# Kernel tuning notes

Measured on AMD Instinct MI355X. Metric: run time of the kernel, lower is better.

Reference implementation:

```python
import jax, jax.numpy as jnp
import numpy as np

H = W = 128
N_RAYS = H * W
N_SAMPLES = 2 ** 21
NUM_LEVELS = 12
BASE_RES = 16
PER_LEVEL_SCALE = 2.0
TABLE_SIZE = 2 ** 19
LEVEL_DIM = 2
RENDER_STEP = 0.005
BG_COLOR = 1.0
PRIMES = (1, 2654435761, 805459861)


def hash_encode(x01, table):
    """Multi-resolution hash-grid encoding. x01: [N,3] in [0,1]; table: [L,T,D]."""
    L, T, D = table.shape
    mask = np.uint32(T - 1)
    feats = []
    for l in range(L):
        res = int(np.ceil(BASE_RES * PER_LEVEL_SCALE ** l))
        pos = x01 * (res - 1)            # [N,3]
        p0f = jnp.floor(pos)
        f = pos - p0f                    # trilinear fractions
        p0 = p0f.astype(jnp.uint32)
        acc = jnp.zeros((x01.shape[0], D), dtype=table.dtype)
        for cx in range(2):
            for cy in range(2):
                for cz in range(2):
                    ix = p0[:, 0] + jnp.uint32(cx)
                    iy = p0[:, 1] + jnp.uint32(cy)
                    iz = p0[:, 2] + jnp.uint32(cz)
                    idx = ((ix * jnp.uint32(PRIMES[0]))
                           ^ (iy * jnp.uint32(PRIMES[1]))
                           ^ (iz * jnp.uint32(PRIMES[2]))) & mask
                    w = ((f[:, 0] if cx else 1.0 - f[:, 0])
                         * (f[:, 1] if cy else 1.0 - f[:, 1])
                         * (f[:, 2] if cz else 1.0 - f[:, 2]))
                    acc = acc + w[:, None] * table[l][idx]
        feats.append(acc)
    return jnp.concatenate(feats, axis=-1)  # [N, L*D]


@jax.custom_vjp
def trunc_exp(x):
    return jnp.exp(x)

def _te_fwd(x):
    return jnp.exp(x), x

def _te_bwd(x, g):
    return (g * jnp.exp(jnp.clip(x, -15.0, 15.0)),)

trunc_exp.defvjp(_te_fwd, _te_bwd)


def setup_inputs() -> dict:
    key = jax.random.key(0)
    ks = jax.random.split(key, 12)
    rays_o = 0.1 * jax.random.normal(ks[0], (N_RAYS, 3), jnp.float32)
    rd = jax.random.normal(ks[1], (N_RAYS, 3), jnp.float32)
    rays_d = rd / jnp.linalg.norm(rd, axis=-1, keepdims=True)
    t_starts = 0.01 + 1.5 * jax.random.uniform(ks[2], (N_SAMPLES,), jnp.float32)
    t_ends = t_starts + RENDER_STEP
    ray_indices = jnp.sort(jax.random.randint(ks[3], (N_SAMPLES,), 0, N_RAYS)).astype(jnp.int32)
    table_density = 1e-2 * jax.random.normal(ks[4], (NUM_LEVELS, TABLE_SIZE, LEVEL_DIM), jnp.float32)
    table_color = 1e-2 * jax.random.normal(ks[5], (NUM_LEVELS, TABLE_SIZE, LEVEL_DIM), jnp.float32)
    d_in = NUM_LEVELS * LEVEL_DIM
    w_d1 = jax.random.normal(ks[6], (d_in, 32), jnp.float32) / np.sqrt(d_in)
    w_d2 = jax.random.normal(ks[7], (32, 1), jnp.float32) / np.sqrt(32)
    w_c1 = jax.random.normal(ks[8], (d_in, 32), jnp.float32) / np.sqrt(d_in)
    w_c2 = jax.random.normal(ks[9], (32, 3), jnp.float32) / np.sqrt(32)
    return {"rays_o": rays_o, "rays_d": rays_d, "t_starts": t_starts, "t_ends": t_ends,
            "ray_indices": ray_indices, "table_density": table_density, "table_color": table_color,
            "w_d1": w_d1, "w_d2": w_d2, "w_c1": w_c1, "w_c2": w_c2}


def reference(rays_o, rays_d, t_starts, t_ends, ray_indices,
              table_density, table_color, w_d1, w_d2, w_c1, w_c2):
    # sample positions along rays
    t_mid = 0.5 * (t_starts + t_ends)
    xs = rays_o[ray_indices] + rays_d[ray_indices] * t_mid[:, None]     # [N,3]
    x01 = jnp.clip((xs + 1.0) * 0.5, 0.0, 1.0)                          # aabb [-1,1] -> [0,1]

    # density branch: hash encode -> tiny MLP -> trunc_exp
    fd = hash_encode(x01, table_density)                                # [N,24]
    sigma = trunc_exp(jax.nn.relu(fd @ w_d1) @ w_d2)[:, 0]              # [N]

    # color branch: hash encode -> tiny MLP -> sigmoid
    fc = hash_encode(x01, table_color)
    rgb = jax.nn.sigmoid(jax.nn.relu(fc @ w_c1) @ w_c2)                 # [N,3]

    # render_weight_from_density (segment-wise exclusive transmittance)
    s = sigma * (t_ends - t_starts)                                     # [N], >= 0
    e = jnp.cumsum(s) - s                                               # exclusive cumsum, nondecreasing
    e_start = jax.ops.segment_min(e, ray_indices, num_segments=N_RAYS)
    trans = jnp.exp(-(e - e_start[ray_indices]))
    alphas = 1.0 - jnp.exp(-s)
    weights = alphas * trans                                            # [N]

    # accumulate_along_rays
    color = jax.ops.segment_sum(weights[:, None] * rgb, ray_indices, num_segments=N_RAYS)  # [R,3]
    acc = jax.ops.segment_sum(weights, ray_indices, num_segments=N_RAYS)                   # [R]
    color = color + (1.0 - acc)[:, None] * BG_COLOR
    color = jnp.clip(color, 0.0, 1.0).reshape(H, W, 3).transpose(2, 0, 1)
    alpha = jnp.clip(acc, 0.0, 1.0).reshape(H, W)
    return color, alpha
```

## Files before the change

kernel.cpp:

```cpp
#include <hip/hip_runtime.h>
#include <hip/hip_fp16.h>
#include <cstdint>
#include <cstddef>

#define HW_NRAYS 16384
#define NSAMP    (1 << 21)
#define NLEV     12
#define TSZ      (1 << 19)
#define TMASK    (TSZ - 1)
#define DIN      24
#define HDIM     32
#define WS_TAB_QWORDS (NLEV * TSZ)
#define WS_TAB_BYTES  ((size_t)WS_TAB_QWORDS * 8)
#define WS_FEAT_BYTES ((size_t)NLEV * NSAMP * 8)
#define PRIME1 2654435761u
#define PRIME2 805459861u

__device__ __forceinline__ float clamp01f(float v) { return fminf(fmaxf(v, 0.f), 1.f); }

__device__ __forceinline__ uint32_t rne_bf16_lo(uint32_t u) {
    return (u + 0x7fffu + ((u >> 16) & 1u)) >> 16;
}
__device__ __forceinline__ float bf_lo(uint32_t v) { return __uint_as_float(v << 16); }
__device__ __forceinline__ float bf_hi(uint32_t v) { return __uint_as_float(v & 0xffff0000u); }

__global__ __launch_bounds__(256)
void ngp_pack_tables(const float2* __restrict__ tab_d,
                     const float2* __restrict__ tab_c,
                     uint2* __restrict__ ws_tab)
{
    const int stride = gridDim.x * blockDim.x;
    for (int i = blockIdx.x * blockDim.x + threadIdx.x; i < WS_TAB_QWORDS; i += stride) {
        const float2 d = tab_d[i];
        const float2 c = tab_c[i];
        const uint32_t w0 = rne_bf16_lo(__float_as_uint(d.x)) | (rne_bf16_lo(__float_as_uint(d.y)) << 16);
        const uint32_t w1 = rne_bf16_lo(__float_as_uint(c.x)) | (rne_bf16_lo(__float_as_uint(c.y)) << 16);
        ws_tab[i] = make_uint2(w0, w1);
    }
}

union H2U { __half2 h2; uint32_t u; };
union F4H2 { float4 f4; __half2 h2[4]; };

__device__ __forceinline__ void level_hashes(float x, float y, float z, int l,
                                             uint32_t* __restrict__ h,
                                             float* __restrict__ w)
{
    const float res1 = (float)((16 << l) - 1);
    const float px = x * res1, py = y * res1, pz = z * res1;
    const float fxf = floorf(px), fyf = floorf(py), fzf = floorf(pz);
    const uint32_t ix = (uint32_t)fxf, iy = (uint32_t)fyf, iz = (uint32_t)fzf;
    const float fx = px - fxf, fy = py - fyf, fz = pz - fzf;
    const uint32_t hx0 = ix, hx1 = ix + 1u;
    const uint32_t hy0 = iy * PRIME1, hy1 = hy0 + PRIME1;
    const uint32_t hz0 = iz * PRIME2, hz1 = hz0 + PRIME2;
    #pragma unroll
    for (int c = 0; c < 8; ++c) {
        h[c] = ((((c & 1) ? hx1 : hx0) ^ ((c & 2) ? hy1 : hy0) ^ ((c & 4) ? hz1 : hz0)) & TMASK);
        w[c] = ((c & 1) ? fx : 1.f - fx) * ((c & 2) ? fy : 1.f - fy) * ((c & 4) ? fz : 1.f - fz);
    }
}

__global__ __launch_bounds__(256)
void ngp_encode(const float* __restrict__ rays_o,
                const float* __restrict__ rays_d,
                const float* __restrict__ t_starts,
                const float* __restrict__ t_ends,
                const int*   __restrict__ ray_idx,
                const uint2* __restrict__ ws_tab,
                uint2* __restrict__ feat)
{
    const int l = blockIdx.x >> 13;
    const int i = ((blockIdx.x & 8191) << 8) | threadIdx.x;

    const int ridx = ray_idx[i];
    const float tm = 0.5f * (t_starts[i] + t_ends[i]);
    const float x = clamp01f((rays_o[3 * ridx + 0] + rays_d[3 * ridx + 0] * tm + 1.f) * 0.5f);
    const float y = clamp01f((rays_o[3 * ridx + 1] + rays_d[3 * ridx + 1] * tm + 1.f) * 0.5f);
    const float z = clamp01f((rays_o[3 * ridx + 2] + rays_d[3 * ridx + 2] * tm + 1.f) * 0.5f);

    const float res1 = (float)((16 << l) - 1);
    const float px = x * res1, py = y * res1, pz = z * res1;
    const float fxf = floorf(px), fyf = floorf(py), fzf = floorf(pz);
    const uint32_t ix = (uint32_t)fxf, iy = (uint32_t)fyf, iz = (uint32_t)fzf;
    const float fx = px - fxf, fy = py - fyf, fz = pz - fzf;
    const float wx0 = 1.f - fx, wx1 = fx;

    const uint32_t hy0 = iy * PRIME1, hy1 = hy0 + PRIME1;
    const uint32_t hz0 = iz * PRIME2, hz1 = hz0 + PRIME2;

    uint32_t hyz[4];
    float    wyz[4];
    hyz[0] = hy0 ^ hz0; wyz[0] = (1.f - fy) * (1.f - fz);
    hyz[1] = hy1 ^ hz0; wyz[1] = fy * (1.f - fz);
    hyz[2] = hy0 ^ hz1; wyz[2] = (1.f - fy) * fz;
    hyz[3] = hy1 ^ hz1; wyz[3] = fy * fz;

    const uint4* pairs = (const uint4*)(ws_tab + (size_t)l * TSZ);

    float a0 = 0.f, a1 = 0.f, b0 = 0.f, b1 = 0.f;
    #pragma unroll
    for (int k = 0; k < 4; ++k) {
        const uint32_t h0 = (ix        ^ hyz[k]) & TMASK;
        const uint32_t h1 = ((ix + 1u) ^ hyz[k]) & TMASK;
        uint4 q0 = pairs[h0 >> 1];
        uint4 q1 = q0;
        if ((h1 >> 1) != (h0 >> 1)) q1 = pairs[h1 >> 1];
        const uint32_t e0x = (h0 & 1u) ? q0.z : q0.x;
        const uint32_t e0y = (h0 & 1u) ? q0.w : q0.y;
        const uint32_t e1x = (h1 & 1u) ? q1.z : q1.x;
        const uint32_t e1y = (h1 & 1u) ? q1.w : q1.y;
        const float w0 = wx0 * wyz[k], w1 = wx1 * wyz[k];
        a0 += w0 * bf_lo(e0x) + w1 * bf_lo(e1x);
        a1 += w0 * bf_hi(e0x) + w1 * bf_hi(e1x);
        b0 += w0 * bf_lo(e0y) + w1 * bf_lo(e1y);
        b1 += w0 * bf_hi(e0y) + w1 * bf_hi(e1y);
    }

    H2U fD, fC;
    fD.h2 = __floats2half2_rn(a0, a1);
    fC.h2 = __floats2half2_rn(b0, b1);
    const unsigned long long packed = (unsigned long long)fD.u | ((unsigned long long)fC.u << 32);
    __builtin_nontemporal_store(packed, (unsigned long long*)(feat + (size_t)l * NSAMP + i));
}

#define PROC_LEVEL2(FA, FB, LIDX)                                                \
    do {                                                                         \
        H2U fDa, fCa, fDb, fCb;                                                  \
        fDa.u = (FA).x; fCa.u = (FA).y; fDb.u = (FB).x; fCb.u = (FB).y;          \
        const __half2 a0A = __low2half2(fDa.h2), a1A = __high2half2(fDa.h2);     \
        const __half2 b0A = __low2half2(fCa.h2), b1A = __high2half2(fCa.h2);     \
        const __half2 a0B = __low2half2(fDb.h2), a1B = __high2half2(fDb.h2);     \
        const __half2 b0B = __low2half2(fCb.h2), b1B = __high2half2(fCb.h2);     \
        const F4H2* wd0 = (const F4H2*)(s_wd1h + (2 * (LIDX) + 0) * 16);         \
        const F4H2* wd1 = (const F4H2*)(s_wd1h + (2 * (LIDX) + 1) * 16);         \
        const F4H2* wc0 = (const F4H2*)(s_wc1h + (2 * (LIDX) + 0) * 16);         \
        const F4H2* wc1 = (const F4H2*)(s_wc1h + (2 * (LIDX) + 1) * 16);         \
        _Pragma("unroll")                                                        \
        for (int q = 0; q < 4; ++q) {                                            \
            F4H2 u0 = wd0[q], u1 = wd1[q], v0 = wc0[q], v1 = wc1[q];             \
            _Pragma("unroll")                                                    \
            for (int p = 0; p < 4; ++p) {                                        \
                hbD2A[q * 4 + p] = __hfma2(a0A, u0.h2[p],                        \
                                     __hfma2(a1A, u1.h2[p], hbD2A[q * 4 + p]));  \
                hbC2A[q * 4 + p] = __hfma2(b0A, v0.h2[p],                        \
                                     __hfma2(b1A, v1.h2[p], hbC2A[q * 4 + p]));  \
                hbD2B[q * 4 + p] = __hfma2(a0B, u0.h2[p],                        \
                                     __hfma2(a1B, u1.h2[p], hbD2B[q * 4 + p]));  \
                hbC2B[q * 4 + p] = __hfma2(b0B, v0.h2[p],                        \
                                     __hfma2(b1B, v1.h2[p], hbC2B[q * 4 + p]));  \
            }                                                                    \
        }                                                                        \
    } while (0)

#define PROC_LEVEL(FV, LIDX)                                                     \
    do {                                                                         \
        H2U fDu, fCu; fDu.u = (FV).x; fCu.u = (FV).y;                            \
        const __half2 a0h = __low2half2(fDu.h2), a1h = __high2half2(fDu.h2);     \
        const __half2 b0h = __low2half2(fCu.h2), b1h = __high2half2(fCu.h2);     \
        const F4H2* wd0 = (const F4H2*)(s_wd1h + (2 * (LIDX) + 0) * 16);         \
        const F4H2* wd1 = (const F4H2*)(s_wd1h + (2 * (LIDX) + 1) * 16);         \
        const F4H2* wc0 = (const F4H2*)(s_wc1h + (2 * (LIDX) + 0) * 16);         \
        const F4H2* wc1 = (const F4H2*)(s_wc1h + (2 * (LIDX) + 1) * 16);         \
        _Pragma("unroll")                                                        \
        for (int q = 0; q < 4; ++q) {                                            \
            F4H2 u0 = wd0[q], u1 = wd1[q], v0 = wc0[q], v1 = wc1[q];             \
            _Pragma("unroll")                                                    \
            for (int p = 0; p < 4; ++p) {                                        \
                hbD2[q * 4 + p] = __hfma2(a0h, u0.h2[p],                         \
                                    __hfma2(a1h, u1.h2[p], hbD2[q * 4 + p]));    \
                hbC2[q * 4 + p] = __hfma2(b0h, v0.h2[p],                         \
                                    __hfma2(b1h, v1.h2[p], hbC2[q * 4 + p]));    \
            }                                                                    \
        }                                                                        \
    } while (0)

__global__ __launch_bounds__(256)
void ngp_render_feat(const float* __restrict__ t_starts,
                     const float* __restrict__ t_ends,
                     const int*   __restrict__ ray_idx,
                     const uint2* __restrict__ feat,
                     const float* __restrict__ w_d1,
                     const float* __restrict__ w_d2,
                     const float* __restrict__ w_c1,
                     const float* __restrict__ w_c2,
                     float* __restrict__ out)
{
    __shared__ __align__(16) __half2 s_wd1h[DIN * 16];
    __shared__ __align__(16) __half2 s_wc1h[DIN * 16];
    __shared__ __align__(16) float   s_wd2[HDIM];
    __shared__ __align__(16) float   s_wc2[HDIM * 3];

    const int tid = threadIdx.x;
    for (int idx = tid; idx < DIN * 16; idx += 256) {
        const int k = idx >> 4, j2 = idx & 15;
        s_wd1h[idx] = __floats2half2_rn(w_d1[k * HDIM + 2 * j2], w_d1[k * HDIM + 2 * j2 + 1]);
        s_wc1h[idx] = __floats2half2_rn(w_c1[k * HDIM + 2 * j2], w_c1[k * HDIM + 2 * j2 + 1]);
    }
    if (tid < HDIM) s_wd2[tid] = w_d2[tid];
    if (tid < HDIM * 3) s_wc2[tid] = w_c2[tid];
    __syncthreads();

    const int lane = tid & 63;
    const int r = blockIdx.x * 4 + (tid >> 6);

    int lo = 0, hi = NSAMP;
    while (lo < hi) { int m = (lo + hi) >> 1; if (ray_idx[m] < r) lo = m + 1; else hi = m; }
    const int start = lo;
    hi = NSAMP;
    while (lo < hi) { int m = (lo + hi) >> 1; if (ray_idx[m] <= r) lo = m + 1; else hi = m; }
    const int end = lo;

    float carry = 0.f, accw = 0.f, cr = 0.f, cg = 0.f, cb = 0.f;

    for (int base = start; base < end; base += 128) {
        const bool vA = (base + lane) < end;
        const bool vB = (base + 64 + lane) < end;
        const int iA = min(base + lane, end - 1);
        const int iB = min(base + 64 + lane, end - 1);

        const float dtA = t_ends[iA] - t_starts[iA];
        const float dtB = t_ends[iB] - t_starts[iB];

        __half2 hbD2A[16], hbC2A[16], hbD2B[16], hbC2B[16];
        #pragma unroll
        for (int j = 0; j < 16; ++j) {
            hbD2A[j] = __floats2half2_rn(0.f, 0.f);
            hbC2A[j] = __floats2half2_rn(0.f, 0.f);
            hbD2B[j] = __floats2half2_rn(0.f, 0.f);
            hbC2B[j] = __floats2half2_rn(0.f, 0.f);
        }

        const uint2* fplA = feat + iA;
        const uint2* fplB = feat + iB;
        #pragma unroll 1
        for (int lg = 0; lg < NLEV; lg += 4) {
            const uint2 fA0 = fplA[(size_t)(lg + 0) * NSAMP];
            const uint2 fA1 = fplA[(size_t)(lg + 1) * NSAMP];
            const uint2 fA2 = fplA[(size_t)(lg + 2) * NSAMP];
            const uint2 fA3 = fplA[(size_t)(lg + 3) * NSAMP];
            const uint2 fB0 = fplB[(size_t)(lg + 0) * NSAMP];
            const uint2 fB1 = fplB[(size_t)(lg + 1) * NSAMP];
            const uint2 fB2 = fplB[(size_t)(lg + 2) * NSAMP];
            const uint2 fB3 = fplB[(size_t)(lg + 3) * NSAMP];
            PROC_LEVEL2(fA0, fB0, lg + 0);
            PROC_LEVEL2(fA1, fB1, lg + 1);
            PROC_LEVEL2(fA2, fB2, lg + 2);
            PROC_LEVEL2(fA3, fB3, lg + 3);
        }

        float sDA = 0.f, sDB = 0.f;
        #pragma unroll
        for (int j = 0; j < 16; ++j) {
            const float2 fa = __half22float2(hbD2A[j]);
            const float2 fb = __half22float2(hbD2B[j]);
            sDA += fmaxf(fa.x, 0.f) * s_wd2[2 * j] + fmaxf(fa.y, 0.f) * s_wd2[2 * j + 1];
            sDB += fmaxf(fb.x, 0.f) * s_wd2[2 * j] + fmaxf(fb.y, 0.f) * s_wd2[2 * j + 1];
        }
        const float svA = vA ? __expf(sDA) * dtA : 0.f;
        const float svB = vB ? __expf(sDB) * dtB : 0.f;

        float prA = 0.f, pgA = 0.f, pbA = 0.f, prB = 0.f, pgB = 0.f, pbB = 0.f;
        #pragma unroll
        for (int j = 0; j < 16; ++j) {
            const float2 fa = __half22float2(hbC2A[j]);
            const float2 fb = __half22float2(hbC2B[j]);
            const float a0 = fmaxf(fa.x, 0.f), a1 = fmaxf(fa.y, 0.f);
            const float c0 = fmaxf(fb.x, 0.f), c1 = fmaxf(fb.y, 0.f);
            const float w00 = s_wc2[3 * (2 * j) + 0], w10 = s_wc2[3 * (2 * j + 1) + 0];
            const float w01 = s_wc2[3 * (2 * j) + 1], w11 = s_wc2[3 * (2 * j + 1) + 1];
            const float w02 = s_wc2[3 * (2 * j) + 2], w12 = s_wc2[3 * (2 * j + 1) + 2];
            prA += a0 * w00 + a1 * w10;  prB += c0 * w00 + c1 * w10;
            pgA += a0 * w01 + a1 * w11;  pgB += c0 * w01 + c1 * w11;
            pbA += a0 * w02 + a1 * w12;  pbB += c0 * w02 + c1 * w12;
        }
        const float RA = 1.f / (1.f + __expf(-prA));
        const float GA = 1.f / (1.f + __expf(-pgA));
        const float BA = 1.f / (1.f + __expf(-pbA));
        const float RB = 1.f / (1.f + __expf(-prB));
        const float GB = 1.f / (1.f + __expf(-pgB));
        const float BB = 1.f / (1.f + __expf(-pbB));

        float inclA = svA;
        #pragma unroll
        for (int off = 1; off < 64; off <<= 1) {
            float t = __shfl_up(inclA, off);
            if (lane >= off) inclA += t;
        }
        const float eA = carry + (inclA - svA);
        const float wA = vA ? (1.f - __expf(-svA)) * __expf(-eA) : 0.f;
        const float totalA = __shfl(inclA, 63);

        float inclB = svB;
        #pragma unroll
        for (int off = 1; off < 64; off <<= 1) {
            float t = __shfl_up(inclB, off);
            if (lane >= off) inclB += t;
        }
        const float eB = carry + totalA + (inclB - svB);
        const float wB = vB ? (1.f - __expf(-svB)) * __expf(-eB) : 0.f;
        carry += totalA + __shfl(inclB, 63);

        accw += wA + wB;
        cr += wA * RA + wB * RB;
        cg += wA * GA + wB * GB;
        cb += wA * BA + wB * BB;
    }

    #pragma unroll
    for (int off = 32; off > 0; off >>= 1) {
        accw += __shfl_down(accw, off);
        cr   += __shfl_down(cr, off);
        cg   += __shfl_down(cg, off);
        cb   += __shfl_down(cb, off);
    }

    if (lane == 0) {
        const float bgw = 1.f - accw;
        out[0 * HW_NRAYS + r] = clamp01f(cr + bgw);
        out[1 * HW_NRAYS + r] = clamp01f(cg + bgw);
        out[2 * HW_NRAYS + r] = clamp01f(cb + bgw);
        out[3 * HW_NRAYS + r] = clamp01f(accw);
    }
}

__global__ __launch_bounds__(256, 6)
void ngp_render_fast(const float* __restrict__ rays_o,
                     const float* __restrict__ rays_d,
                     const float* __restrict__ t_starts,
                     const float* __restrict__ t_ends,
                     const int*   __restrict__ ray_idx,
                     const uint2* __restrict__ ws_tab,
                     const float* __restrict__ w_d1,
                     const float* __restrict__ w_d2,
                     const float* __restrict__ w_c1,
                     const float* __restrict__ w_c2,
                     float* __restrict__ out)
{
    __shared__ __align__(16) __half2 s_wd1h[DIN * 16];
    __shared__ __align__(16) __half2 s_wc1h[DIN * 16];
    __shared__ __align__(16) float   s_wd2[HDIM];
    __shared__ __align__(16) float   s_wc2[HDIM * 3];
    __shared__ __align__(16) uint2   s_feat[4 * NLEV * 64];

    const int tid = threadIdx.x;
    for (int idx = tid; idx < DIN * 16; idx += 256) {
        const int k = idx >> 4, j2 = idx & 15;
        s_wd1h[idx] = __floats2half2_rn(w_d1[k * HDIM + 2 * j2], w_d1[k * HDIM + 2 * j2 + 1]);
        s_wc1h[idx] = __floats2half2_rn(w_c1[k * HDIM + 2 * j2], w_c1[k * HDIM + 2 * j2 + 1]);
    }
    if (tid < HDIM) s_wd2[tid] = w_d2[tid];
    if (tid < HDIM * 3) s_wc2[tid] = w_c2[tid];
    __syncthreads();

    const int lane = tid & 63;
    const int wv = tid >> 6;
    const int r = blockIdx.x * 4 + wv;
    uint2* const feat = s_feat + wv * (NLEV * 64) + lane;

    int lo = 0, hi = NSAMP;
    while (lo < hi) { int m = (lo + hi) >> 1; if (ray_idx[m] < r) lo = m + 1; else hi = m; }
    const int start = lo;
    hi = NSAMP;
    while (lo < hi) { int m = (lo + hi) >> 1; if (ray_idx[m] <= r) lo = m + 1; else hi = m; }
    const int end = lo;

    const float ox = rays_o[3 * r + 0], oy = rays_o[3 * r + 1], oz = rays_o[3 * r + 2];
    const float dx = rays_d[3 * r + 0], dy = rays_d[3 * r + 1], dz = rays_d[3 * r + 2];

    float carry = 0.f, accw = 0.f, cr = 0.f, cg = 0.f, cb = 0.f;

    for (int base = start; base < end; base += 64) {
        const int i = base + lane;
        const bool valid = i < end;
        float sv = 0.f, R = 0.f, G = 0.f, B = 0.f;
        if (valid) {
            const float ts = t_starts[i], te = t_ends[i];
            const float tm = 0.5f * (ts + te);
            const float x01x = clamp01f((ox + dx * tm + 1.f) * 0.5f);
            const float x01y = clamp01f((oy + dy * tm + 1.f) * 0.5f);
            const float x01z = clamp01f((oz + dz * tm + 1.f) * 0.5f);

            #pragma unroll 1
            for (int l = 0; l < NLEV; ++l) {
                uint32_t h[8]; float w[8];
                level_hashes(x01x, x01y, x01z, l, h, w);
                const uint2* tl = ws_tab + (size_t)l * TSZ;
                float a0 = 0.f, a1 = 0.f, b0 = 0.f, b1 = 0.f;
                #pragma unroll
                for (int c = 0; c < 8; ++c) {
                    const uint2 v = tl[h[c]];
                    a0 += w[c] * bf_lo(v.x); a1 += w[c] * bf_hi(v.x);
                    b0 += w[c] * bf_lo(v.y); b1 += w[c] * bf_hi(v.y);
                }
                H2U fD, fC;
                fD.h2 = __floats2half2_rn(a0, a1);
                fC.h2 = __floats2half2_rn(b0, b1);
                feat[l * 64] = make_uint2(fD.u, fC.u);
            }

            __half2 hbD2[16], hbC2[16];
            #pragma unroll
            for (int j = 0; j < 16; ++j) {
                hbD2[j] = __floats2half2_rn(0.f, 0.f);
                hbC2[j] = __floats2half2_rn(0.f, 0.f);
            }

            #pragma unroll
            for (int l = 0; l < NLEV; ++l) {
                const uint2 fv = feat[l * 64];
                PROC_LEVEL(fv, l);
            }

            float sD = 0.f;
            #pragma unroll
            for (int j = 0; j < 16; ++j) {
                const float2 f = __half22float2(hbD2[j]);
                sD += fmaxf(f.x, 0.f) * s_wd2[2 * j] + fmaxf(f.y, 0.f) * s_wd2[2 * j + 1];
            }
            sv = __expf(sD) * (te - ts);

            float pr = 0.f, pg = 0.f, pb = 0.f;
            #pragma unroll
            for (int j = 0; j < 16; ++j) {
                const float2 f = __half22float2(hbC2[j]);
                const float h0 = fmaxf(f.x, 0.f), h1 = fmaxf(f.y, 0.f);
                pr += h0 * s_wc2[3 * (2 * j) + 0] + h1 * s_wc2[3 * (2 * j + 1) + 0];
                pg += h0 * s_wc2[3 * (2 * j) + 1] + h1 * s_wc2[3 * (2 * j + 1) + 1];
                pb += h0 * s_wc2[3 * (2 * j) + 2] + h1 * s_wc2[3 * (2 * j + 1) + 2];
            }
            R = 1.f / (1.f + __expf(-pr));
            G = 1.f / (1.f + __expf(-pg));
            B = 1.f / (1.f + __expf(-pb));
        }

        float incl = sv;
        #pragma unroll
        for (int off = 1; off < 64; off <<= 1) {
            float t = __shfl_up(incl, off);
            if (lane >= off) incl += t;
        }
        const float e = carry + (incl - sv);
        const float w = valid ? (1.f - __expf(-sv)) * __expf(-e) : 0.f;
        accw += w; cr += w * R; cg += w * G; cb += w * B;
        carry += __shfl(incl, 63);
    }

    #pragma unroll
    for (int off = 32; off > 0; off >>= 1) {
        accw += __shfl_down(accw, off);
        cr   += __shfl_down(cr, off);
        cg   += __shfl_down(cg, off);
        cb   += __shfl_down(cb, off);
    }

    if (lane == 0) {
        const float bgw = 1.f - accw;
        out[0 * HW_NRAYS + r] = clamp01f(cr + bgw);
        out[1 * HW_NRAYS + r] = clamp01f(cg + bgw);
        out[2 * HW_NRAYS + r] = clamp01f(cb + bgw);
        out[3 * HW_NRAYS + r] = clamp01f(accw);
    }
}

__global__ __launch_bounds__(64, 4)
void ngp_render_ref(const float* __restrict__ rays_o,
                    const float* __restrict__ rays_d,
                    const float* __restrict__ t_starts,
                    const float* __restrict__ t_ends,
                    const int*   __restrict__ ray_idx,
                    const float* __restrict__ tab_d,
                    const float* __restrict__ tab_c,
                    const float* __restrict__ w_d1,
                    const float* __restrict__ w_d2,
                    const float* __restrict__ w_c1,
                    const float* __restrict__ w_c2,
                    float* __restrict__ out)
{
    __shared__ __align__(16) float s_wd1[DIN * HDIM];
    __shared__ __align__(16) float s_wc1[DIN * HDIM];
    __shared__ __align__(16) float s_wd2[HDIM];
    __shared__ __align__(16) float s_wc2[HDIM * 3];

    const int lane = threadIdx.x;
    for (int i = lane; i < DIN * HDIM; i += 64) { s_wd1[i] = w_d1[i]; s_wc1[i] = w_c1[i]; }
    if (lane < HDIM) s_wd2[lane] = w_d2[lane];
    for (int i = lane; i < HDIM * 3; i += 64) s_wc2[i] = w_c2[i];
    __syncthreads();

    const int r = blockIdx.x;
    int lo = 0, hi = NSAMP;
    while (lo < hi) { int m = (lo + hi) >> 1; if (ray_idx[m] < r) lo = m + 1; else hi = m; }
    const int start = lo;
    hi = NSAMP;
    while (lo < hi) { int m = (lo + hi) >> 1; if (ray_idx[m] <= r) lo = m + 1; else hi = m; }
    const int end = lo;

    const float ox = rays_o[3 * r + 0], oy = rays_o[3 * r + 1], oz = rays_o[3 * r + 2];
    const float dx = rays_d[3 * r + 0], dy = rays_d[3 * r + 1], dz = rays_d[3 * r + 2];

    float carry = 0.f, accw = 0.f, cr = 0.f, cg = 0.f, cb = 0.f;

    for (int base = start; base < end; base += 64) {
        const int i = base + lane;
        const bool valid = i < end;
        float sv = 0.f, R = 0.f, G = 0.f, B = 0.f;
        if (valid) {
            const float ts = t_starts[i], te = t_ends[i];
            const float tm = 0.5f * (ts + te);
            const float x01x = clamp01f((ox + dx * tm + 1.f) * 0.5f);
            const float x01y = clamp01f((oy + dy * tm + 1.f) * 0.5f);
            const float x01z = clamp01f((oz + dz * tm + 1.f) * 0.5f);

            float hbD[HDIM], hbC[HDIM];
            #pragma unroll
            for (int j = 0; j < HDIM; ++j) { hbD[j] = 0.f; hbC[j] = 0.f; }

            #pragma unroll 1
            for (int l = 0; l < NLEV; ++l) {
                uint32_t h[8]; float w[8];
                level_hashes(x01x, x01y, x01z, l, h, w);
                const float* td = tab_d + (size_t)l * (TSZ * 2);
                const float* tc = tab_c + (size_t)l * (TSZ * 2);
                float a0 = 0.f, a1 = 0.f, b0 = 0.f, b1 = 0.f;
                #pragma unroll
                for (int c = 0; c < 8; ++c) {
                    const float2 vd = *(const float2*)(td + (size_t)(h[c] * 2u));
                    const float2 vc = *(const float2*)(tc + (size_t)(h[c] * 2u));
                    a0 += w[c] * vd.x; a1 += w[c] * vd.y; b0 += w[c] * vc.x; b1 += w[c] * vc.y;
                }
                #pragma unroll
                for (int j = 0; j < HDIM; j += 4) {
                    const float4 u0 = *(const float4*)(s_wd1 + (2 * l + 0) * HDIM + j);
                    const float4 u1 = *(const float4*)(s_wd1 + (2 * l + 1) * HDIM + j);
                    hbD[j + 0] += a0 * u0.x + a1 * u1.x;
                    hbD[j + 1] += a0 * u0.y + a1 * u1.y;
                    hbD[j + 2] += a0 * u0.z + a1 * u1.z;
                    hbD[j + 3] += a0 * u0.w + a1 * u1.w;
                    const float4 v0 = *(const float4*)(s_wc1 + (2 * l + 0) * HDIM + j);
                    const float4 v1 = *(const float4*)(s_wc1 + (2 * l + 1) * HDIM + j);
                    hbC[j + 0] += b0 * v0.x + b1 * v1.x;
                    hbC[j + 1] += b0 * v0.y + b1 * v1.y;
                    hbC[j + 2] += b0 * v0.z + b1 * v1.z;
                    hbC[j + 3] += b0 * v0.w + b1 * v1.w;
                }
            }

            float dotv = 0.f;
            #pragma unroll
            for (int j = 0; j < HDIM; ++j) dotv += fmaxf(hbD[j], 0.f) * s_wd2[j];
            sv = __expf(dotv) * (te - ts);

            float pr = 0.f, pg = 0.f, pb = 0.f;
            #pragma unroll
            for (int j = 0; j < HDIM; ++j) {
                const float hj = fmaxf(hbC[j], 0.f);
                pr += hj * s_wc2[3 * j + 0];
                pg += hj * s_wc2[3 * j + 1];
                pb += hj * s_wc2[3 * j + 2];
            }
            R = 1.f / (1.f + __expf(-pr));
            G = 1.f / (1.f + __expf(-pg));
            B = 1.f / (1.f + __expf(-pb));
        }

        float incl = sv;
        #pragma unroll
        for (int off = 1; off < 64; off <<= 1) {
            float t = __shfl_up(incl, off);
            if (lane >= off) incl += t;
        }
        const float e = carry + (incl - sv);
        const float w = valid ? (1.f - __expf(-sv)) * __expf(-e) : 0.f;
        accw += w; cr += w * R; cg += w * G; cb += w * B;
        carry += __shfl(incl, 63);
    }

    #pragma unroll
    for (int off = 32; off > 0; off >>= 1) {
        accw += __shfl_down(accw, off);
        cr   += __shfl_down(cr, off);
        cg   += __shfl_down(cg, off);
        cb   += __shfl_down(cb, off);
    }

    if (lane == 0) {
        const float bgw = 1.f - accw;
        out[0 * HW_NRAYS + r] = clamp01f(cr + bgw);
        out[1 * HW_NRAYS + r] = clamp01f(cg + bgw);
        out[2 * HW_NRAYS + r] = clamp01f(cb + bgw);
        out[3 * HW_NRAYS + r] = clamp01f(accw);
    }
}

extern "C" void kernel_launch(void* const* d_in, const int* in_sizes, int n_in,
                              void* d_out, int out_size, void* d_ws, size_t ws_size,
                              hipStream_t stream) {
    const float* rays_o        = (const float*)d_in[0];
    const float* rays_d        = (const float*)d_in[1];
    const float* t_starts      = (const float*)d_in[2];
    const float* t_ends        = (const float*)d_in[3];
    const int*   ray_indices   = (const int*)d_in[4];
    const float* table_density = (const float*)d_in[5];
    const float* table_color   = (const float*)d_in[6];
    const float* w_d1          = (const float*)d_in[7];
    const float* w_d2          = (const float*)d_in[8];
    const float* w_c1          = (const float*)d_in[9];
    const float* w_c2          = (const float*)d_in[10];
    float* outp = (float*)d_out;

    if (ws_size >= WS_TAB_BYTES + WS_FEAT_BYTES) {
        uint2* ws_tab = (uint2*)d_ws;
        uint2* ws_feat = (uint2*)((char*)d_ws + WS_TAB_BYTES);
        hipLaunchKernelGGL(ngp_pack_tables, dim3(4096), dim3(256), 0, stream,
                           (const float2*)table_density, (const float2*)table_color, ws_tab);
        hipLaunchKernelGGL(ngp_encode, dim3(NLEV * (NSAMP / 256)), dim3(256), 0, stream,
                           rays_o, rays_d, t_starts, t_ends, ray_indices, ws_tab, ws_feat);
        hipLaunchKernelGGL(ngp_render_feat, dim3(HW_NRAYS / 4), dim3(256), 0, stream,
                           t_starts, t_ends, ray_indices, ws_feat,
                           w_d1, w_d2, w_c1, w_c2, outp);
    } else if (ws_size >= WS_TAB_BYTES) {
        uint2* ws_tab = (uint2*)d_ws;
        hipLaunchKernelGGL(ngp_pack_tables, dim3(4096), dim3(256), 0, stream,
                           (const float2*)table_density, (const float2*)table_color, ws_tab);
        hipLaunchKernelGGL(ngp_render_fast, dim3(HW_NRAYS / 4), dim3(256), 0, stream,
                           rays_o, rays_d, t_starts, t_ends, ray_indices, ws_tab,
                           w_d1, w_d2, w_c1, w_c2, outp);
    } else {
        hipLaunchKernelGGL(ngp_render_ref, dim3(HW_NRAYS), dim3(64), 0, stream,
                           rays_o, rays_d, t_starts, t_ends, ray_indices,
                           table_density, table_color,
                           w_d1, w_d2, w_c1, w_c2, outp);
    }
}
```

Baseline: 980.2 us.

## Split feature buffer into density and color planes, process branches sequentially

The encode kernel now writes density and color features into two separate 32-bit planes instead of one interleaved 64-bit record. The render kernel runs the density MLP pass and the color MLP pass one after the other, each with its own 16-register half2 accumulator pair. This halves the live accumulator set at any moment and is meant to lower register pressure and raise occupancy. The cost is twice as many narrower global loads and two separate streaming passes over the feature planes.

Result: faster. 849.7 us (-13.3%).

```diff
diff --git a/kernel.cpp b/kernel.cpp
--- a/kernel.cpp
+++ b/kernel.cpp
@@ -68,7 +68,7 @@
                 const float* __restrict__ t_ends,
                 const int*   __restrict__ ray_idx,
                 const uint2* __restrict__ ws_tab,
-                uint2* __restrict__ feat)
+                uint32_t* __restrict__ featd)
 {
     const int l = blockIdx.x >> 13;
     const int i = ((blockIdx.x & 8191) << 8) | threadIdx.x;
@@ -120,35 +120,26 @@
     H2U fD, fC;
     fD.h2 = __floats2half2_rn(a0, a1);
     fC.h2 = __floats2half2_rn(b0, b1);
-    const unsigned long long packed = (unsigned long long)fD.u | ((unsigned long long)fC.u << 32);
-    __builtin_nontemporal_store(packed, (unsigned long long*)(feat + (size_t)l * NSAMP + i));
-}
-
-#define PROC_LEVEL2(FA, FB, LIDX)                                                \
+    __builtin_nontemporal_store(fD.u, featd + (size_t)l * NSAMP + i);
+    __builtin_nontemporal_store(fC.u, featd + (size_t)(NLEV + l) * NSAMP + i);
+}
+
+#define PROC2(WBASE, FA, FB, LIDX)                                               \
     do {                                                                         \
-        H2U fDa, fCa, fDb, fCb;                                                  \
-        fDa.u = (FA).x; fCa.u = (FA).y; fDb.u = (FB).x; fCb.u = (FB).y;          \
-        const __half2 a0A = __low2half2(fDa.h2), a1A = __high2half2(fDa.h2);     \
-        const __half2 b0A = __low2half2(fCa.h2), b1A = __high2half2(fCa.h2);     \
-        const __half2 a0B = __low2half2(fDb.h2), a1B = __high2half2(fDb.h2);     \
-        const __half2 b0B = __low2half2(fCb.h2), b1B = __high2half2(fCb.h2);     \
-        const F4H2* wd0 = (const F4H2*)(s_wd1h + (2 * (LIDX) + 0) * 16);         \
-        const F4H2* wd1 = (const F4H2*)(s_wd1h + (2 * (LIDX) + 1) * 16);         \
-        const F4H2* wc0 = (const F4H2*)(s_wc1h + (2 * (LIDX) + 0) * 16);         \
-        const F4H2* wc1 = (const F4H2*)(s_wc1h + (2 * (LIDX) + 1) * 16);         \
+        H2U fa, fb; fa.u = (FA); fb.u = (FB);                                    \
+        const __half2 a0A = __low2half2(fa.h2), a1A = __high2half2(fa.h2);       \
+        const __half2 a0B = __low2half2(fb.h2), a1B = __high2half2(fb.h2);       \
+        const F4H2* w0 = (const F4H2*)((WBASE) + (2 * (LIDX) + 0) * 16);         \
+        const F4H2* w1 = (const F4H2*)((WBASE) + (2 * (LIDX) + 1) * 16);         \
         _Pragma("unroll")                                                        \
         for (int q = 0; q < 4; ++q) {                                            \
-            F4H2 u0 = wd0[q], u1 = wd1[q], v0 = wc0[q], v1 = wc1[q];             \
+            F4H2 u0 = w0[q], u1 = w1[q];                                         \
             _Pragma("unroll")                                                    \
             for (int p = 0; p < 4; ++p) {                                        \
-                hbD2A[q * 4 + p] = __hfma2(a0A, u0.h2[p],                        \
-                                     __hfma2(a1A, u1.h2[p], hbD2A[q * 4 + p]));  \
-                hbC2A[q * 4 + p] = __hfma2(b0A, v0.h2[p],                        \
-                                     __hfma2(b1A, v1.h2[p], hbC2A[q * 4 + p]));  \
-                hbD2B[q * 4 + p] = __hfma2(a0B, u0.h2[p],                        \
-                                     __hfma2(a1B, u1.h2[p], hbD2B[q * 4 + p]));  \
-                hbC2B[q * 4 + p] = __hfma2(b0B, v0.h2[p],                        \
-                                     __hfma2(b1B, v1.h2[p], hbC2B[q * 4 + p]));  \
+                accA[q * 4 + p] = __hfma2(a0A, u0.h2[p],                         \
+                                    __hfma2(a1A, u1.h2[p], accA[q * 4 + p]));    \
+                accB[q * 4 + p] = __hfma2(a0B, u0.h2[p],                         \
+                                    __hfma2(a1B, u1.h2[p], accB[q * 4 + p]));    \
             }                                                                    \
         }                                                                        \
     } while (0)
@@ -179,7 +170,7 @@
 void ngp_render_feat(const float* __restrict__ t_starts,
                      const float* __restrict__ t_ends,
                      const int*   __restrict__ ray_idx,
-                     const uint2* __restrict__ feat,
+                     const uint32_t* __restrict__ featd,
                      const float* __restrict__ w_d1,
                      const float* __restrict__ w_d2,
                      const float* __restrict__ w_c1,
@@ -203,6 +194,7 @@
 
     const int lane = tid & 63;
     const int r = blockIdx.x * 4 + (tid >> 6);
+    const uint32_t* featc = featd + (size_t)NLEV * NSAMP;
 
     int lo = 0, hi = NSAMP;
     while (lo < hi) { int m = (lo + hi) >> 1; if (ray_idx[m] < r) lo = m + 1; else hi = m; }
@@ -222,64 +214,89 @@
         const float dtA = t_ends[iA] - t_starts[iA];
         const float dtB = t_ends[iB] - t_starts[iB];
 
-        __half2 hbD2A[16], hbC2A[16], hbD2B[16], hbC2B[16];
-        #pragma unroll
-        for (int j = 0; j < 16; ++j) {
-            hbD2A[j] = __floats2half2_rn(0.f, 0.f);
-            hbC2A[j] = __floats2half2_rn(0.f, 0.f);
-            hbD2B[j] = __floats2half2_rn(0.f, 0.f);
-            hbC2B[j] = __floats2half2_rn(0.f, 0.f);
-        }
-
-        const uint2* fplA = feat + iA;
-        const uint2* fplB = feat + iB;
-        #pragma unroll 1
-        for (int lg = 0; lg < NLEV; lg += 4) {
-            const uint2 fA0 = fplA[(size_t)(lg + 0) * NSAMP];
-            const uint2 fA1 = fplA[(size_t)(lg + 1) * NSAMP];
-            const uint2 fA2 = fplA[(size_t)(lg + 2) * NSAMP];
-            const uint2 fA3 = fplA[(size_t)(lg + 3) * NSAMP];
-            const uint2 fB0 = fplB[(size_t)(lg + 0) * NSAMP];
-            const uint2 fB1 = fplB[(size_t)(lg + 1) * NSAMP];
-            const uint2 fB2 = fplB[(size_t)(lg + 2) * NSAMP];
-            const uint2 fB3 = fplB[(size_t)(lg + 3) * NSAMP];
-            PROC_LEVEL2(fA0, fB0, lg + 0);
-            PROC_LEVEL2(fA1, fB1, lg + 1);
-            PROC_LEVEL2(fA2, fB2, lg + 2);
-            PROC_LEVEL2(fA3, fB3, lg + 3);
-        }
-
-        float sDA = 0.f, sDB = 0.f;
-        #pragma unroll
-        for (int j = 0; j < 16; ++j) {
-            const float2 fa = __half22float2(hbD2A[j]);
-            const float2 fb = __half22float2(hbD2B[j]);
-            sDA += fmaxf(fa.x, 0.f) * s_wd2[2 * j] + fmaxf(fa.y, 0.f) * s_wd2[2 * j + 1];
-            sDB += fmaxf(fb.x, 0.f) * s_wd2[2 * j] + fmaxf(fb.y, 0.f) * s_wd2[2 * j + 1];
-        }
-        const float svA = vA ? __expf(sDA) * dtA : 0.f;
-        const float svB = vB ? __expf(sDB) * dtB : 0.f;
-
-        float prA = 0.f, pgA = 0.f, pbA = 0.f, prB = 0.f, pgB = 0.f, pbB = 0.f;
-        #pragma unroll
-        for (int j = 0; j < 16; ++j) {
-            const float2 fa = __half22float2(hbC2A[j]);
-            const float2 fb = __half22float2(hbC2B[j]);
-            const float a0 = fmaxf(fa.x, 0.f), a1 = fmaxf(fa.y, 0.f);
-            const float c0 = fmaxf(fb.x, 0.f), c1 = fmaxf(fb.y, 0.f);
-            const float w00 = s_wc2[3 * (2 * j) + 0], w10 = s_wc2[3 * (2 * j + 1) + 0];
-            const float w01 = s_wc2[3 * (2 * j) + 1], w11 = s_wc2[3 * (2 * j + 1) + 1];
-            const float w02 = s_wc2[3 * (2 * j) + 2], w12 = s_wc2[3 * (2 * j + 1) + 2];
-            prA += a0 * w00 + a1 * w10;  prB += c0 * w00 + c1 * w10;
-            pgA += a0 * w01 + a1 * w11;  pgB += c0 * w01 + c1 * w11;
-            pbA += a0 * w02 + a1 * w12;  pbB += c0 * w02 + c1 * w12;
-        }
-        const float RA = 1.f / (1.f + __expf(-prA));
-        const float GA = 1.f / (1.f + __expf(-pgA));
-        const float BA = 1.f / (1.f + __expf(-pbA));
-        const float RB = 1.f / (1.f + __expf(-prB));
-        const float GB = 1.f / (1.f + __expf(-pgB));
-        const float BB = 1.f / (1.f + __expf(-pbB));
+        float svA, svB;
+        {
+            __half2 accA[16], accB[16];
+            #pragma unroll
+            for (int j = 0; j < 16; ++j) {
+                accA[j] = __floats2half2_rn(0.f, 0.f);
+                accB[j] = __floats2half2_rn(0.f, 0.f);
+            }
+            const uint32_t* fA = featd + iA;
+            const uint32_t* fB = featd + iB;
+            #pragma unroll 1
+            for (int lg = 0; lg < NLEV; lg += 4) {
+                const uint32_t a0 = fA[(size_t)(lg + 0) * NSAMP];
+                const uint32_t a1 = fA[(size_t)(lg + 1) * NSAMP];
+                const uint32_t a2 = fA[(size_t)(lg + 2) * NSAMP];
+                const uint32_t a3 = fA[(size_t)(lg + 3) * NSAMP];
+                const uint32_t b0 = fB[(size_t)(lg + 0) * NSAMP];
+                const uint32_t b1 = fB[(size_t)(lg + 1) * NSAMP];
+                const uint32_t b2 = fB[(size_t)(lg + 2) * NSAMP];
+                const uint32_t b3 = fB[(size_t)(lg + 3) * NSAMP];
+                PROC2(s_wd1h, a0, b0, lg + 0);
+                PROC2(s_wd1h, a1, b1, lg + 1);
+                PROC2(s_wd1h, a2, b2, lg + 2);
+                PROC2(s_wd1h, a3, b3, lg + 3);
+            }
+            float sDA = 0.f, sDB = 0.f;
+            #pragma unroll
+            for (int j = 0; j < 16; ++j) {
+                const float2 fa = __half22float2(accA[j]);
+                const float2 fb = __half22float2(accB[j]);
+                sDA += fmaxf(fa.x, 0.f) * s_wd2[2 * j] + fmaxf(fa.y, 0.f) * s_wd2[2 * j + 1];
+                sDB += fmaxf(fb.x, 0.f) * s_wd2[2 * j] + fmaxf(fb.y, 0.f) * s_wd2[2 * j + 1];
+            }
+            svA = vA ? __expf(sDA) * dtA : 0.f;
+            svB = vB ? __expf(sDB) * dtB : 0.f;
+        }
+
+        float RA, GA, BA, RB, GB, BB;
+        {
+            __half2 accA[16], accB[16];
+            #pragma unroll
+            for (int j = 0; j < 16; ++j) {
+                accA[j] = __floats2half2_rn(0.f, 0.f);
+                accB[j] = __floats2half2_rn(0.f, 0.f);
+            }
+            const uint32_t* fA = featc + iA;
+            const uint32_t* fB = featc + iB;
+            #pragma unroll 1
+            for (int lg = 0; lg < NLEV; lg += 4) {
+                const uint32_t a0 = fA[(size_t)(lg + 0) * NSAMP];
+                const uint32_t a1 = fA[(size_t)(lg + 1) * NSAMP];
+                const uint32_t a2 = fA[(size_t)(lg + 2) * NSAMP];
+                const uint32_t a3 = fA[(size_t)(lg + 3) * NSAMP];
+                const uint32_t b0 = fB[(size_t)(lg + 0) * NSAMP];
+                const uint32_t b1 = fB[(size_t)(lg + 1) * NSAMP];
+                const uint32_t b2 = fB[(size_t)(lg + 2) * NSAMP];
+                const uint32_t b3 = fB[(size_t)(lg + 3) * NSAMP];
+                PROC2(s_wc1h, a0, b0, lg + 0);
+                PROC2(s_wc1h, a1, b1, lg + 1);
+                PROC2(s_wc1h, a2, b2, lg + 2);
+                PROC2(s_wc1h, a3, b3, lg + 3);
+            }
+            float prA = 0.f, pgA = 0.f, pbA = 0.f, prB = 0.f, pgB = 0.f, pbB = 0.f;
+            #pragma unroll
+            for (int j = 0; j < 16; ++j) {
+                const float2 fa = __half22float2(accA[j]);
+                const float2 fb = __half22float2(accB[j]);
+                const float a0 = fmaxf(fa.x, 0.f), a1 = fmaxf(fa.y, 0.f);
+                const float c0 = fmaxf(fb.x, 0.f), c1 = fmaxf(fb.y, 0.f);
+                const float w00 = s_wc2[3 * (2 * j) + 0], w10 = s_wc2[3 * (2 * j + 1) + 0];
+                const float w01 = s_wc2[3 * (2 * j) + 1], w11 = s_wc2[3 * (2 * j + 1) + 1];
+                const float w02 = s_wc2[3 * (2 * j) + 2], w12 = s_wc2[3 * (2 * j + 1) + 2];
+                prA += a0 * w00 + a1 * w10;  prB += c0 * w00 + c1 * w10;
+                pgA += a0 * w01 + a1 * w11;  pgB += c0 * w01 + c1 * w11;
+                pbA += a0 * w02 + a1 * w12;  pbB += c0 * w02 + c1 * w12;
+            }
+            RA = 1.f / (1.f + __expf(-prA));
+            GA = 1.f / (1.f + __expf(-pgA));
+            BA = 1.f / (1.f + __expf(-pbA));
+            RB = 1.f / (1.f + __expf(-prB));
+            GB = 1.f / (1.f + __expf(-pgB));
+            BB = 1.f / (1.f + __expf(-pbB));
+        }
 
         float inclA = svA;
         #pragma unroll
@@ -611,13 +628,13 @@
 
     if (ws_size >= WS_TAB_BYTES + WS_FEAT_BYTES) {
         uint2* ws_tab = (uint2*)d_ws;
-        uint2* ws_feat = (uint2*)((char*)d_ws + WS_TAB_BYTES);
+        uint32_t* ws_featd = (uint32_t*)((char*)d_ws + WS_TAB_BYTES);
         hipLaunchKernelGGL(ngp_pack_tables, dim3(4096), dim3(256), 0, stream,
                            (const float2*)table_density, (const float2*)table_color, ws_tab);
         hipLaunchKernelGGL(ngp_encode, dim3(NLEV * (NSAMP / 256)), dim3(256), 0, stream,
-                           rays_o, rays_d, t_starts, t_ends, ray_indices, ws_tab, ws_feat);
+                           rays_o, rays_d, t_starts, t_ends, ray_indices, ws_tab, ws_featd);
         hipLaunchKernelGGL(ngp_render_feat, dim3(HW_NRAYS / 4), dim3(256), 0, stream,
-                           t_starts, t_ends, ray_indices, ws_feat,
+                           t_starts, t_ends, ray_indices, ws_featd,
                            w_d1, w_d2, w_c1, w_c2, outp);
     } else if (ws_size >= WS_TAB_BYTES) {
         uint2* ws_tab = (uint2*)d_ws;
```
